# Kernel tuning notes

Measured on AMD Instinct MI355X. Metric: run time of the kernel, lower is better.

The kernel has to match this reference:

```python
import jax, jax.numpy as jnp
import numpy as np

B, N, D = 8, 900, 256
SA_H, CA_H = 8, 8
L, P = 4, 4
FF = 2048
SHAPES = ((128, 128), (64, 64), (32, 32), (16, 16))
STARTS = (0, 16384, 20480, 21504)
S = 21760
D_BAND = (D // 6) * 2   # 84
D_ROPE = 3 * D_BAND     # 252
NF = D_BAND // 2        # 42
EPS = 1e-5


def _ln(x, g, b):
    mu = jnp.mean(x, -1, keepdims=True)
    var = jnp.mean((x - mu) ** 2, -1, keepdims=True)
    return (x - mu) * jax.lax.rsqrt(var + EPS) * g + b


def _rotate_half(x):
    x1 = x[..., 0::2]
    x2 = x[..., 1::2]
    return jnp.stack([-x2, x1], axis=-1).reshape(x.shape)


def _rope(q, k, boxes):
    freqs = 1.0 / (10000.0 ** (jnp.arange(NF, dtype=jnp.float32) / NF))
    cx, cy = boxes[..., 0], boxes[..., 1]
    xy = cx * cy

    def cs(v, f):
        a = v[..., None] * f
        return jnp.repeat(jnp.cos(a), 2, -1), jnp.repeat(jnp.sin(a), 2, -1)

    cx_c, cx_s = cs(cx, freqs)
    cy_c, cy_s = cs(cy, freqs)
    xy_c, xy_s = cs(xy, freqs * 0.1)
    cos = jnp.concatenate([cx_c, cy_c, xy_c], -1)
    sin = jnp.concatenate([cx_s, cy_s, xy_s], -1)

    def app(t):
        a, rest = t[..., :D_ROPE], t[..., D_ROPE:]
        return jnp.concatenate([a * cos + _rotate_half(a) * sin, rest], -1)

    return app(q), app(k)


def _bilinear(img, xy):
    # img: (Hl, Wl, C); xy: (M, 2) normalized in [0,1]
    # torch grid_sample semantics: align_corners=False, zero padding
    Hl, Wl, _ = img.shape
    x = xy[:, 0] * Wl - 0.5
    y = xy[:, 1] * Hl - 0.5
    x0 = jnp.floor(x)
    y0 = jnp.floor(y)
    lx = x - x0
    ly = y - y0
    x0i = x0.astype(jnp.int32)
    y0i = y0.astype(jnp.int32)

    def tap(yi, xi):
        valid = (xi >= 0) & (xi < Wl) & (yi >= 0) & (yi < Hl)
        v = img[jnp.clip(yi, 0, Hl - 1), jnp.clip(xi, 0, Wl - 1)]
        return v * valid[:, None].astype(v.dtype)

    return (tap(y0i, x0i) * ((1 - ly) * (1 - lx))[:, None]
            + tap(y0i, x0i + 1) * ((1 - ly) * lx)[:, None]
            + tap(y0i + 1, x0i) * (ly * (1 - lx))[:, None]
            + tap(y0i + 1, x0i + 1) * (ly * lx)[:, None])


def _forward(tgt, memory, query_pos, ref_boxes, reference_points,
             wq, bq, wk, bk, wv, bv, sa_wo, sa_bo, n1_g, n1_b,
             off_w, off_b, aw_w, aw_b, val_w, val_b, co_w, co_b,
             n2_g, n2_b, ff1_w, ff1_b, ff2_w, ff2_b, n3_g, n3_b):
    dh = D // SA_H
    # --- self attention with ComplexRoPE2D applied pre-projection ---
    q = tgt + query_pos
    k = tgt + query_pos
    q, k = _rope(q, k, ref_boxes)
    qh = (q @ wq + bq).reshape(B, N, SA_H, dh).transpose(0, 2, 1, 3)
    kh = (k @ wk + bk).reshape(B, N, SA_H, dh).transpose(0, 2, 1, 3)
    vh = (tgt @ wv + bv).reshape(B, N, SA_H, dh).transpose(0, 2, 1, 3)
    att = jax.nn.softmax(jnp.einsum('bhqd,bhkd->bhqk', qh, kh) * (dh ** -0.5), axis=-1)
    sa = jnp.einsum('bhqk,bhkd->bhqd', att, vh).transpose(0, 2, 1, 3).reshape(B, N, D)
    tgt = _ln(tgt + sa @ sa_wo + sa_bo, n1_g, n1_b)

    # --- multi-scale deformable cross-attention ---
    cdh = D // CA_H
    q2 = tgt + query_pos
    value = (memory @ val_w + val_b).reshape(B, S, CA_H, cdh)
    off = (q2 @ off_w + off_b).reshape(B, N, CA_H, L, P, 2)
    aw = jax.nn.softmax((q2 @ aw_w + aw_b).reshape(B, N, CA_H, L * P), axis=-1)
    aw = aw.reshape(B, N, CA_H, L, P)
    # offset normalizer is (W, H) per level
    normalizer = jnp.array([[w_, h_] for (h_, w_) in SHAPES], dtype=jnp.float32)
    loc = reference_points[:, :, None, :, None, :] + off / normalizer[None, None, None, :, None, :]
    out = jnp.zeros((B, CA_H, N, cdh), dtype=tgt.dtype)
    for l, (Hl, Wl) in enumerate(SHAPES):
        st = STARTS[l]
        v_l = value[:, st:st + Hl * Wl].reshape(B, Hl, Wl, CA_H, cdh)
        v_l = v_l.transpose(0, 3, 1, 2, 4).reshape(B * CA_H, Hl, Wl, cdh)
        loc_l = loc[:, :, :, l].transpose(0, 2, 1, 3, 4).reshape(B * CA_H, N * P, 2)
        s_l = jax.vmap(_bilinear)(v_l, loc_l).reshape(B, CA_H, N, P, cdh)
        out = out + jnp.einsum('bhnpd,bnhp->bhnd', s_l, aw[:, :, :, l])
    ca = out.transpose(0, 2, 1, 3).reshape(B, N, D) @ co_w + co_b
    tgt = _ln(tgt + ca, n2_g, n2_b)

    # --- FFN ---
    ff = jax.nn.relu(tgt @ ff1_w + ff1_b) @ ff2_w + ff2_b
    return _ln(tgt + ff, n3_g, n3_b)


def setup_inputs() -> dict:
    key = jax.random.key(0)
    ks = jax.random.split(key, 16)

    def wmat(k, shape):
        return jax.random.normal(k, shape, jnp.float32) * 0.02

    z = lambda *s: jnp.zeros(s, jnp.float32)
    o = lambda *s: jnp.ones(s, jnp.float32)
    return dict(
        tgt=jax.random.normal(ks[0], (B, N, D), jnp.float32),
        memory=jax.random.normal(ks[1], (B, S, D), jnp.float32),
        query_pos=jax.random.normal(ks[2], (B, N, D), jnp.float32) * 0.02,
        ref_boxes=jax.random.uniform(ks[3], (B, N, 4), jnp.float32),
        reference_points=jax.random.uniform(ks[4], (B, N, L, 2), jnp.float32),
        wq=wmat(ks[5], (D, D)), bq=z(D),
        wk=wmat(ks[6], (D, D)), bk=z(D),
        wv=wmat(ks[7], (D, D)), bv=z(D),
        sa_wo=wmat(ks[8], (D, D)), sa_bo=z(D),
        n1_g=o(D), n1_b=z(D),
        off_w=wmat(ks[9], (D, CA_H * L * P * 2)), off_b=z(CA_H * L * P * 2),
        aw_w=wmat(ks[10], (D, CA_H * L * P)), aw_b=z(CA_H * L * P),
        val_w=wmat(ks[11], (D, D)), val_b=z(D),
        co_w=wmat(ks[12], (D, D)), co_b=z(D),
        n2_g=o(D), n2_b=z(D),
        ff1_w=wmat(ks[13], (D, FF)), ff1_b=z(FF),
        ff2_w=wmat(ks[14], (FF, D)), ff2_b=z(D),
        n3_g=o(D), n3_b=z(D))


def reference(tgt, memory, query_pos, ref_boxes, reference_points,
              wq, bq, wk, bk, wv, bv, sa_wo, sa_bo, n1_g, n1_b,
              off_w, off_b, aw_w, aw_b, val_w, val_b, co_w, co_b,
              n2_g, n2_b, ff1_w, ff1_b, ff2_w, ff2_b, n3_g, n3_b):
    return _forward(tgt, memory, query_pos, ref_boxes, reference_points,
                    wq, bq, wk, bk, wv, bv, sa_wo, sa_bo, n1_g, n1_b,
                    off_w, off_b, aw_w, aw_b, val_w, val_b, co_w, co_b,
                    n2_g, n2_b, ff1_w, ff1_b, ff2_w, ff2_b, n3_g, n3_b)
```

## Files before the change

### kernel.cpp

```cpp
#include <hip/hip_runtime.h>
#include <hip/hip_bf16.h>
#include <math.h>

#define B_ 8
#define N_ 900
#define D_ 256
#define S_ 21760
#define H_ 8
#define DH 32
#define FF_ 2048
#define NROWS (B_*N_)

typedef __attribute__((ext_vector_type(8))) short bf16x8;
typedef __attribute__((ext_vector_type(4))) float f32x4;

union BU { bf16x8 v; short s[8]; unsigned long long u[2]; };

static __device__ inline short f2bf_s(float x) {
  __hip_bfloat16 h = __float2bfloat16(x);
  return *reinterpret_cast<short*>(&h);
}

__device__ __forceinline__ void gload_lds16(const float* g, float* lds) {
  __builtin_amdgcn_global_load_lds(
      (const __attribute__((address_space(1))) void*)g,
      (__attribute__((address_space(3))) void*)lds, 16, 0, 0);
}

__global__ __launch_bounds__(128) void rope_kernel(
    const float* __restrict__ tgt, const float* __restrict__ qpos,
    const float* __restrict__ boxes, __hip_bfloat16* __restrict__ out)
{
  int row = blockIdx.x;
  int tid = threadIdx.x;
  const float* x = tgt  + (size_t)row * D_;
  const float* p = qpos + (size_t)row * D_;
  float a0 = x[2*tid]   + p[2*tid];
  float a1 = x[2*tid+1] + p[2*tid+1];
  float o0 = a0, o1 = a1;
  if (tid < 126) {
    int band = tid / 42;
    int fi   = tid - band * 42;
    float freq = powf(10000.0f, -(float)fi / 42.0f);
    float cx = boxes[(size_t)row*4 + 0];
    float cy = boxes[(size_t)row*4 + 1];
    float v  = (band == 0) ? cx : (band == 1 ? cy : cx * cy);
    if (band == 2) freq *= 0.1f;
    float ang = v * freq;
    float c = cosf(ang), s = sinf(ang);
    o0 = a0 * c - a1 * s;
    o1 = a1 * c + a0 * s;
  }
  short2 sv = make_short2(f2bf_s(o0), f2bf_s(o1));
  *(short2*)&out[(size_t)row*D_ + 2*tid] = sv;
}

__global__ __launch_bounds__(256) void wtrans_kernel(
    const float* __restrict__ wq, const float* __restrict__ wk,
    const float* __restrict__ wv, const float* __restrict__ sa_wo,
    const float* __restrict__ offw, const float* __restrict__ valw,
    const float* __restrict__ cow, const float* __restrict__ aww,
    const float* __restrict__ ff1w, const float* __restrict__ ff2w,
    short* __restrict__ Wt)
{
  int bid = blockIdx.x;
  const float* W; short* out; int K, N, tile;
  if (bid < 448) {
    int wi = bid >> 6; tile = bid & 63; K = 256; N = 256;
    const float* tab[7] = {wq, wk, wv, sa_wo, offw, valw, cow};
    const int   off[7]  = {0, 65536, 131072, 196608, 262144, 360448, 425984};
    W = tab[wi]; out = Wt + off[wi];
  } else if (bid < 480) {
    tile = bid - 448; K = 256; N = 128; W = aww; out = Wt + 327680;
  } else if (bid < 992) {
    tile = bid - 480; K = 256; N = 2048; W = ff1w; out = Wt + 491520;
  } else {
    tile = bid - 992; K = 2048; N = 256; W = ff2w; out = Wt + 1015808;
  }
  int ntn = N >> 5;
  int tk = tile / ntn, tn = tile - tk * ntn;
  __shared__ float t[32][33];
  int c = threadIdx.x & 31, rr = threadIdx.x >> 5;
  #pragma unroll
  for (int i = 0; i < 4; ++i)
    t[rr + i*8][c] = W[(size_t)(tk*32 + rr + i*8) * N + tn*32 + c];
  __syncthreads();
  #pragma unroll
  for (int i = 0; i < 4; ++i)
    out[(size_t)(tn*32 + rr + i*8) * K + tk*32 + c] = f2bf_s(t[c][rr + i*8]);
}

template<int BM, int KK, bool ABF16, bool A2ADD, bool RELU, int OUTMODE>
__global__ __launch_bounds__(256) void mgemm_kernel(
    const void* __restrict__ Ap, const float* __restrict__ A2p,
    const short* __restrict__ Wt,
    const float* __restrict__ bias, const float* __restrict__ bias2,
    void* __restrict__ Cp, void* __restrict__ Cp2, int M, int N,
    const float* __restrict__ Xres, const float* __restrict__ lng,
    const float* __restrict__ lnb)
{
  constexpr int MS = BM / 16;
  constexpr bool SWAP = (OUTMODE != 2);
  __shared__ short As[BM * 256];
  int tid = threadIdx.x;
  int w = tid >> 6, lane = tid & 63;
  int g = lane >> 4, r = lane & 15;
  int m0 = blockIdx.x * BM;
  int nw = blockIdx.y * 256 + w * 64;
  bool active = nw < N;

  f32x4 acc[MS][4];
  #pragma unroll
  for (int i = 0; i < MS; ++i)
    #pragma unroll
    for (int j = 0; j < 4; ++j) acc[i][j] = (f32x4){0.f,0.f,0.f,0.f};

  for (int kb = 0; kb < KK; kb += 256) {
    if (KK > 256 && kb) __syncthreads();
    #pragma unroll
    for (int i = 0; i < BM/8; ++i) {
      int u = i*256 + tid;
      int row = u >> 5, c8 = u & 31;
      BU pk;
      if (ABF16) {
        pk.v = *(const bf16x8*)((const short*)Ap + (size_t)(m0+row)*KK + kb + c8*8);
      } else {
        const float* ap = (const float*)Ap + (size_t)(m0+row)*KK + kb + c8*8;
        float4 a0 = *(const float4*)ap;
        float4 a1 = *(const float4*)(ap + 4);
        if (A2ADD) {
          const float* a2 = A2p + (size_t)(m0+row)*KK + kb + c8*8;
          float4 b0 = *(const float4*)a2;
          float4 b1 = *(const float4*)(a2 + 4);
          a0.x += b0.x; a0.y += b0.y; a0.z += b0.z; a0.w += b0.w;
          a1.x += b1.x; a1.y += b1.y; a1.z += b1.z; a1.w += b1.w;
        }
        pk.s[0]=f2bf_s(a0.x); pk.s[1]=f2bf_s(a0.y); pk.s[2]=f2bf_s(a0.z); pk.s[3]=f2bf_s(a0.w);
        pk.s[4]=f2bf_s(a1.x); pk.s[5]=f2bf_s(a1.y); pk.s[6]=f2bf_s(a1.z); pk.s[7]=f2bf_s(a1.w);
      }
      int col = (c8*8) ^ ((row & 7) << 3);
      *(bf16x8*)&As[row*256 + col] = pk.v;
    }
    __syncthreads();
    if (active) {
      #pragma unroll
      for (int kk = 0; kk < 8; ++kk) {
        BU bfr[4];
        #pragma unroll
        for (int ns = 0; ns < 4; ++ns) {
          const short* wp = Wt + (size_t)(nw + ns*16 + r)*KK + kb + kk*32;
          bfr[ns].u[0] = *(const unsigned long long*)(wp + 4*g);
          bfr[ns].u[1] = *(const unsigned long long*)(wp + 16 + 4*g);
        }
        #pragma unroll
        for (int ms = 0; ms < MS; ++ms) {
          int row = ms*16 + r;
          int c0 = (kk*32 + g*4)      ^ ((r & 7) << 3);
          int c1 = (kk*32 + 16 + g*4) ^ ((r & 7) << 3);
          BU af;
          af.u[0] = *(const unsigned long long*)&As[row*256 + c0];
          af.u[1] = *(const unsigned long long*)&As[row*256 + c1];
          #pragma unroll
          for (int ns = 0; ns < 4; ++ns) {
            if (SWAP)
              acc[ms][ns] = __builtin_amdgcn_mfma_f32_16x16x32_bf16(
                  bfr[ns].v, af.v, acc[ms][ns], 0, 0, 0);
            else
              acc[ms][ns] = __builtin_amdgcn_mfma_f32_16x16x32_bf16(
                  af.v, bfr[ns].v, acc[ms][ns], 0, 0, 0);
          }
        }
      }
    }
  }

  if (OUTMODE == 5) {
    float vv[MS][16];
    float ps[MS], pq[MS];
    #pragma unroll
    for (int ms = 0; ms < MS; ++ms) {
      ps[ms] = 0.f; pq[ms] = 0.f;
      int m = m0 + ms*16 + r;
      #pragma unroll
      for (int ns = 0; ns < 4; ++ns) {
        int n0 = nw + ns*16 + g*4;
        float4 b4 = *(const float4*)&bias[n0];
        float4 x4 = *(const float4*)&Xres[(size_t)m*256 + n0];
        #pragma unroll
        for (int j = 0; j < 4; ++j) {
          float v = acc[ms][ns][j] + ((const float*)&b4)[j] + ((const float*)&x4)[j];
          vv[ms][ns*4 + j] = v;
          ps[ms] += v; pq[ms] += v*v;
        }
      }
      ps[ms] += __shfl_xor(ps[ms], 16); ps[ms] += __shfl_xor(ps[ms], 32);
      pq[ms] += __shfl_xor(pq[ms], 16); pq[ms] += __shfl_xor(pq[ms], 32);
    }
    __syncthreads();
    float* red = (float*)As;
    if (g == 0) {
      #pragma unroll
      for (int ms = 0; ms < MS; ++ms) {
        red[(ms*16 + r)*8 + w]     = ps[ms];
        red[(ms*16 + r)*8 + 4 + w] = pq[ms];
      }
    }
    __syncthreads();
    #pragma unroll
    for (int ms = 0; ms < MS; ++ms) {
      int rowi = ms*16 + r;
      float ts = red[rowi*8+0]+red[rowi*8+1]+red[rowi*8+2]+red[rowi*8+3];
      float tq = red[rowi*8+4]+red[rowi*8+5]+red[rowi*8+6]+red[rowi*8+7];
      float mu = ts * (1.0f/256.0f);
      float var = tq * (1.0f/256.0f) - mu*mu;
      float rs = rsqrtf(fmaxf(var, 0.f) + 1e-5f);
      int m = m0 + ms*16 + r;
      #pragma unroll
      for (int ns = 0; ns < 4; ++ns) {
        int n0 = nw + ns*16 + g*4;
        float4 g4 = *(const float4*)&lng[n0];
        float4 be = *(const float4*)&lnb[n0];
        float4 ov;
        ov.x = (vv[ms][ns*4+0] - mu)*rs*g4.x + be.x;
        ov.y = (vv[ms][ns*4+1] - mu)*rs*g4.y + be.y;
        ov.z = (vv[ms][ns*4+2] - mu)*rs*g4.z + be.z;
        ov.w = (vv[ms][ns*4+3] - mu)*rs*g4.w + be.w;
        *(float4*)&((float*)Cp)[(size_t)m*256 + n0] = ov;
      }
    }
    return;
  }

  if (!active) return;

  #pragma unroll
  for (int ms = 0; ms < MS; ++ms) {
    #pragma unroll
    for (int ns = 0; ns < 4; ++ns) {
      if (SWAP) {
        int n0 = nw + ns*16 + g*4;
        int m  = m0 + ms*16 + r;
        float4 b4;
        if (OUTMODE == 3 || OUTMODE == 4)
          b4 = (n0 < 256) ? *(const float4*)&bias[n0]
                          : *(const float4*)&bias2[n0 - 256];
        else
          b4 = *(const float4*)&bias[n0];
        float v0 = acc[ms][ns][0] + b4.x;
        float v1 = acc[ms][ns][1] + b4.y;
        float v2 = acc[ms][ns][2] + b4.z;
        float v3 = acc[ms][ns][3] + b4.w;
        if (RELU) {
          v0 = fmaxf(v0, 0.f); v1 = fmaxf(v1, 0.f);
          v2 = fmaxf(v2, 0.f); v3 = fmaxf(v3, 0.f);
        }
        if (OUTMODE == 0) {
          *(float4*)&((float*)Cp)[(size_t)m*N + n0] = make_float4(v0,v1,v2,v3);
        } else if (OUTMODE == 1) {
          short4 sv = make_short4(f2bf_s(v0), f2bf_s(v1), f2bf_s(v2), f2bf_s(v3));
          *(short4*)&((short*)Cp)[(size_t)m*N + n0] = sv;
        } else if (OUTMODE == 3) {
          short4 sv = make_short4(f2bf_s(v0), f2bf_s(v1), f2bf_s(v2), f2bf_s(v3));
          if (n0 < 256) *(short4*)&((short*)Cp )[(size_t)m*256 + n0]       = sv;
          else          *(short4*)&((short*)Cp2)[(size_t)m*256 + (n0-256)] = sv;
        } else {
          float4 fv = make_float4(v0,v1,v2,v3);
          if (n0 < 256) *(float4*)&((float*)Cp )[(size_t)m*256 + n0]       = fv;
          else          *(float4*)&((float*)Cp2)[(size_t)m*128 + (n0-256)] = fv;
        }
      } else {
        int n = nw + ns*16 + r;
        float bsc = bias[n];
        int hh = n >> 5, dd = n & 31;
        int mb = m0 + ms*16 + g*4;
        short4 sv = make_short4(
            f2bf_s(acc[ms][ns][0] + bsc), f2bf_s(acc[ms][ns][1] + bsc),
            f2bf_s(acc[ms][ns][2] + bsc), f2bf_s(acc[ms][ns][3] + bsc));
        int bb = mb / N_, bbe = (mb + 3) / N_;
        if (bb == bbe) {
          int nn = mb - bb * N_;
          *(short4*)&((short*)Cp)[((size_t)((bb*H_ + hh)*DH + dd))*N_ + nn] = sv;
        } else {
          const short* sp = (const short*)&sv;
          #pragma unroll
          for (int j = 0; j < 4; ++j) {
            int m = mb + j;
            int b2 = m / N_, nn = m - b2 * N_;
            ((short*)Cp)[((size_t)((b2*H_ + hh)*DH + dd))*N_ + nn] = sp[j];
          }
        }
      }
    }
  }
}

__global__ __launch_bounds__(256) void vgemm_kernel(
    const float* __restrict__ Ap, const short* __restrict__ Wt,
    const float* __restrict__ bias, short* __restrict__ Cp)
{
  __shared__ float buf[8][1024];
  __shared__ float dump[1024];
  int tid = threadIdx.x;
  int w = tid >> 6, l = tid & 63;
  int g = l >> 4, r = l & 15;
  int nw = w * 64;

  BU wreg[4][8];
  #pragma unroll
  for (int ns = 0; ns < 4; ++ns) {
    const short* wp = Wt + (size_t)(nw + ns*16 + r) * 256;
    #pragma unroll
    for (int kk = 0; kk < 8; ++kk) {
      wreg[ns][kk].u[0] = *(const unsigned long long*)(wp + kk*32 + 4*g);
      wreg[ns][kk].u[1] = *(const unsigned long long*)(wp + kk*32 + 16 + 4*g);
    }
  }
  float4 bs4[4];
  #pragma unroll
  for (int ns = 0; ns < 4; ++ns) bs4[ns] = *(const float4*)&bias[nw + ns*16 + g*4];

  int srow = w*8 + (l >> 3);
  int schunk = (l & 7) ^ (srow & 7);
  const float* gbase = Ap + ((size_t)blockIdx.x*160 + srow) * 256 + schunk*4;

  #pragma unroll
  for (int t = 0; t < 6; ++t)
    gload_lds16(gbase + (t>>3)*8192 + (t&7)*32, &buf[t][w*256]);

  f32x4 acc[2][4];
  #pragma unroll
  for (int i = 0; i < 2; ++i)
    #pragma unroll
    for (int j = 0; j < 4; ++j) acc[i][j] = (f32x4){0.f,0.f,0.f,0.f};

  int bb = blockIdx.x / 136;
  int pixblk = (blockIdx.x % 136) * 160;

  for (int s = 0; s < 5; ++s) {
    #pragma unroll
    for (int c = 0; c < 8; ++c) {
      int t = s*8 + c;
      int tn = t + 6;
      if (tn < 40) gload_lds16(gbase + (tn>>3)*8192 + (tn&7)*32,
                               &buf[(c+6)&7][w*256]);
      else         gload_lds16(gbase, &dump[w*256]);
      asm volatile("s_waitcnt vmcnt(6)" ::: "memory");
      __builtin_amdgcn_s_barrier();
      const float* bp = &buf[c][0];
      #pragma unroll
      for (int ms = 0; ms < 2; ++ms) {
        int row = ms*16 + r;
        const float* rp = bp + row*32;
        float4 f0 = *(const float4*)&rp[((g    ) ^ (row & 7)) * 4];
        float4 f1 = *(const float4*)&rp[((g + 4) ^ (row & 7)) * 4];
        BU af;
        af.s[0]=f2bf_s(f0.x); af.s[1]=f2bf_s(f0.y); af.s[2]=f2bf_s(f0.z); af.s[3]=f2bf_s(f0.w);
        af.s[4]=f2bf_s(f1.x); af.s[5]=f2bf_s(f1.y); af.s[6]=f2bf_s(f1.z); af.s[7]=f2bf_s(f1.w);
        #pragma unroll
        for (int ns = 0; ns < 4; ++ns)
          acc[ms][ns] = __builtin_amdgcn_mfma_f32_16x16x32_bf16(
              wreg[ns][c].v, af.v, acc[ms][ns], 0, 0, 0);
      }
    }
    int pix0 = pixblk + s*32;
    #pragma unroll
    for (int ms = 0; ms < 2; ++ms) {
      #pragma unroll
      for (int ns = 0; ns < 4; ++ns) {
        int pix = pix0 + ms*16 + r;
        int n0  = nw + ns*16 + g*4;
        int hh = n0 >> 5, dd = n0 & 31;
        short4 sv = make_short4(
            f2bf_s(acc[ms][ns][0] + bs4[ns].x),
            f2bf_s(acc[ms][ns][1] + bs4[ns].y),
            f2bf_s(acc[ms][ns][2] + bs4[ns].z),
            f2bf_s(acc[ms][ns][3] + bs4[ns].w));
        *(short4*)&Cp[((size_t)(bb*H_ + hh)*S_ + pix)*32 + dd] = sv;
        acc[ms][ns] = (f32x4){0.f,0.f,0.f,0.f};
      }
    }
  }
}

__global__ __launch_bounds__(64) void mfma_attn_kernel(
    const __hip_bfloat16* __restrict__ Q,
    const __hip_bfloat16* __restrict__ K,
    const __hip_bfloat16* __restrict__ Vt,
    float* __restrict__ O)
{
  const int NQT = 29;
  int wid = blockIdx.x;
  int qt = wid % NQT, bh = wid / NQT;
  int b = bh >> 3, h = bh & 7;
  int lane = threadIdx.x;
  int g = lane >> 4, r = lane & 15;
  int q0 = qt * 32;
  const float scale = 0.17677669529663687f;

  union U { bf16x8 v; short s[8]; unsigned long long u64[2]; };

  U qf[2];
  #pragma unroll
  for (int qq = 0; qq < 2; ++qq) {
    int qrow = min(q0 + qq*16 + r, N_ - 1);
    const __hip_bfloat16* qp = Q + ((size_t)(b*N_ + qrow))*D_ + h*DH;
    qf[qq].u64[0] = *(const unsigned long long*)(qp + 4*g);
    qf[qq].u64[1] = *(const unsigned long long*)(qp + 16 + 4*g);
  }

  f32x4 oaccA[2], oaccB[2];
  #pragma unroll
  for (int qq = 0; qq < 2; ++qq) {
    oaccA[qq] = (f32x4){0.f,0.f,0.f,0.f};
    oaccB[qq] = (f32x4){0.f,0.f,0.f,0.f};
  }
  float m0v = -1e30f, m1v = -1e30f, l0v = 0.f, l1v = 0.f;
  const f32x4 zero = {0.f,0.f,0.f,0.f};

  const __hip_bfloat16* vbase0 = Vt + (size_t)(bh*DH + r) * N_;
  const __hip_bfloat16* vbase1 = Vt + (size_t)(bh*DH + 16 + r) * N_;

  for (int kt = 0; kt < N_; kt += 32) {
    U kf0, kf1;
    {
      int kr0 = min(kt + r, N_ - 1);
      int kr1 = min(kt + 16 + r, N_ - 1);
      const __hip_bfloat16* kp0 = K + ((size_t)(b*N_ + kr0))*D_ + h*DH;
      const __hip_bfloat16* kp1 = K + ((size_t)(b*N_ + kr1))*D_ + h*DH;
      kf0.u64[0] = *(const unsigned long long*)(kp0 + 4*g);
      kf0.u64[1] = *(const unsigned long long*)(kp0 + 16 + 4*g);
      kf1.u64[0] = *(const unsigned long long*)(kp1 + 4*g);
      kf1.u64[1] = *(const unsigned long long*)(kp1 + 16 + 4*g);
    }
    U vf0, vf1;
    vf0.u64[0] = *(const unsigned long long*)(vbase0 + kt + 4*g);
    vf0.u64[1] = *(const unsigned long long*)(vbase0 + kt + 16 + 4*g);
    vf1.u64[0] = *(const unsigned long long*)(vbase1 + kt + 4*g);
    vf1.u64[1] = *(const unsigned long long*)(vbase1 + kt + 16 + 4*g);

    #pragma unroll
    for (int qq = 0; qq < 2; ++qq) {
      f32x4 s0 = __builtin_amdgcn_mfma_f32_16x16x32_bf16(kf0.v, qf[qq].v, zero, 0, 0, 0);
      f32x4 s1 = __builtin_amdgcn_mfma_f32_16x16x32_bf16(kf1.v, qf[qq].v, zero, 0, 0, 0);
      float m = qq ? m1v : m0v;
      float lv = qq ? l1v : l0v;

      float sc[8];
      #pragma unroll
      for (int j = 0; j < 4; ++j) {
        sc[j]   = (kt + 4*g + j      < N_) ? s0[j] * scale : -1e30f;
        sc[4+j] = (kt + 16 + 4*g + j < N_) ? s1[j] * scale : -1e30f;
      }
      float mx = sc[0];
      #pragma unroll
      for (int j = 1; j < 8; ++j) mx = fmaxf(mx, sc[j]);
      mx = fmaxf(mx, __shfl_xor(mx, 16));
      mx = fmaxf(mx, __shfl_xor(mx, 32));

      float mnew = fmaxf(m, mx);
      float corr = __expf(m - mnew);
      float p[8], ps = 0.f;
      #pragma unroll
      for (int j = 0; j < 8; ++j) { p[j] = __expf(sc[j] - mnew); ps += p[j]; }
      ps += __shfl_xor(ps, 16);
      ps += __shfl_xor(ps, 32);
      lv = lv * corr + ps;
      if (qq) { m1v = mnew; l1v = lv; } else { m0v = mnew; l0v = lv; }
      #pragma unroll
      for (int j = 0; j < 4; ++j) { oaccA[qq][j] *= corr; oaccB[qq][j] *= corr; }

      U pf;
      #pragma unroll
      for (int j = 0; j < 8; ++j) pf.s[j] = f2bf_s(p[j]);

      oaccA[qq] = __builtin_amdgcn_mfma_f32_16x16x32_bf16(vf0.v, pf.v, oaccA[qq], 0, 0, 0);
      oaccB[qq] = __builtin_amdgcn_mfma_f32_16x16x32_bf16(vf1.v, pf.v, oaccB[qq], 0, 0, 0);
    }
  }

  #pragma unroll
  for (int qq = 0; qq < 2; ++qq) {
    int qrow = q0 + qq*16 + r;
    if (qrow < N_) {
      float inv = 1.0f / (qq ? l1v : l0v);
      float* op = O + ((size_t)(b*N_ + qrow))*D_ + h*DH;
      #pragma unroll
      for (int j = 0; j < 4; ++j) {
        op[4*g + j]      = oaccA[qq][j] * inv;
        op[16 + 4*g + j] = oaccB[qq][j] * inv;
      }
    }
  }
}

__global__ __launch_bounds__(256) void sample4_kernel(
    const __hip_bfloat16* __restrict__ V, const float* __restrict__ offp,
    const float* __restrict__ awl, const float* __restrict__ refp,
    float* __restrict__ out)
{
  int tid = threadIdx.x;
  int q = tid >> 6, t = tid & 63;
  int row = blockIdx.x * 4 + q;
  int b = row / N_;
  __shared__ float s_aw[4][128];
  __shared__ float s_loc[4][256];
  #pragma unroll
  for (int i = 0; i < 2; ++i)
    s_aw[q][t + i*64] = awl[(size_t)row*128 + t + i*64];
  {
    const float norms[4] = {128.f, 64.f, 32.f, 16.f};
    #pragma unroll
    for (int i = 0; i < 4; ++i) {
      int e = t + i*64;
      int rem = e & 31, li = rem >> 3, ax = rem & 1;
      s_loc[q][e] = refp[((size_t)row*4 + li)*2 + ax]
                  + offp[(size_t)row*256 + e] / norms[li];
    }
  }
  __syncthreads();
  if (t < 8) {
    float mx = -1e30f;
    for (int j = 0; j < 16; ++j) mx = fmaxf(mx, s_aw[q][t*16+j]);
    float sum = 0.f;
    for (int j = 0; j < 16; ++j) sum += __expf(s_aw[q][t*16+j] - mx);
    float inv = 1.0f / sum;
    for (int j = 0; j < 16; ++j)
      s_aw[q][t*16+j] = __expf(s_aw[q][t*16+j] - mx) * inv;
  }
  __syncthreads();
  int h = t >> 3, dq = t & 7;
  const int dims[4]   = {128, 64, 32, 16};
  const int starts[4] = {0, 16384, 20480, 21504};
  const __hip_bfloat16* Vb = V + ((size_t)(b*H_ + h) * S_) * 32 + dq*4;
  float a0 = 0.f, a1 = 0.f, a2 = 0.f, a3 = 0.f;
  #pragma unroll
  for (int l = 0; l < 4; ++l) {
    int Wl = dims[l], st = starts[l];
    #pragma unroll
    for (int p = 0; p < 4; ++p) {
      float lx = s_loc[q][h*32 + l*8 + p*2 + 0];
      float ly = s_loc[q][h*32 + l*8 + p*2 + 1];
      float x = lx * Wl - 0.5f, y = ly * Wl - 0.5f;
      float x0f = floorf(x), y0f = floorf(y);
      float fx = x - x0f, fy = y - y0f;
      int x0 = (int)x0f, y0 = (int)y0f;
      float v0 = 0.f, v1 = 0.f, v2 = 0.f, v3 = 0.f;
      #pragma unroll
      for (int ty = 0; ty < 2; ++ty) {
        int yi = y0 + ty;
        float wy = ty ? fy : (1.f - fy);
        if (yi < 0 || yi >= Wl) continue;
        #pragma unroll
        for (int txi = 0; txi < 2; ++txi) {
          int xi = x0 + txi;
          float wx = txi ? fx : (1.f - fx);
          if (xi < 0 || xi >= Wl) continue;
          unsigned long long vv =
              *(const unsigned long long*)&Vb[(size_t)(st + yi*Wl + xi) * 32];
          float ww = wy * wx;
          v0 += ww * __uint_as_float((unsigned)(vv) << 16);
          v1 += ww * __uint_as_float((unsigned)(vv) & 0xffff0000u);
          v2 += ww * __uint_as_float((unsigned)(vv >> 32) << 16);
          v3 += ww * __uint_as_float((unsigned)(vv >> 32) & 0xffff0000u);
        }
      }
      float aw = s_aw[q][h*16 + l*4 + p];
      a0 += aw * v0; a1 += aw * v1; a2 += aw * v2; a3 += aw * v3;
    }
  }
  float4 res = make_float4(a0, a1, a2, a3);
  *(float4*)&out[(size_t)row*D_ + h*DH + dq*4] = res;
}

extern "C" void kernel_launch(void* const* d_in, const int* in_sizes, int n_in,
                              void* d_out, int out_size, void* d_ws, size_t ws_size,
                              hipStream_t stream)
{
  const float* tgt    = (const float*)d_in[0];
  const float* memory = (const float*)d_in[1];
  const float* qpos   = (const float*)d_in[2];
  const float* boxes  = (const float*)d_in[3];
  const float* refp   = (const float*)d_in[4];
  const float* wq = (const float*)d_in[5];   const float* bq = (const float*)d_in[6];
  const float* wk = (const float*)d_in[7];   const float* bk = (const float*)d_in[8];
  const float* wv = (const float*)d_in[9];   const float* bv = (const float*)d_in[10];
  const float* sa_wo = (const float*)d_in[11]; const float* sa_bo = (const float*)d_in[12];
  const float* n1g = (const float*)d_in[13]; const float* n1b = (const float*)d_in[14];
  const float* off_w = (const float*)d_in[15]; const float* off_b = (const float*)d_in[16];
  const float* aw_w  = (const float*)d_in[17]; const float* aw_b  = (const float*)d_in[18];
  const float* val_w = (const float*)d_in[19]; const float* val_b = (const float*)d_in[20];
  const float* co_w  = (const float*)d_in[21]; const float* co_b  = (const float*)d_in[22];
  const float* n2g = (const float*)d_in[23]; const float* n2b = (const float*)d_in[24];
  const float* ff1_w = (const float*)d_in[25]; const float* ff1_b = (const float*)d_in[26];
  const float* ff2_w = (const float*)d_in[27]; const float* ff2_b = (const float*)d_in[28];
  const float* n3g = (const float*)d_in[29]; const float* n3b = (const float*)d_in[30];

  char* ws = (char*)d_ws;
  size_t NE = (size_t)NROWS * D_;
  __hip_bfloat16* Vv = (__hip_bfloat16*)ws;
  __hip_bfloat16* FFM = (__hip_bfloat16*)ws;
  size_t p = (size_t)B_ * S_ * D_ * sizeof(__hip_bfloat16);
  float* A  = (float*)(ws + p); p += NE*4;
  float* Qb = (float*)(ws + p); p += NE*4;
  float* Kb = (float*)(ws + p); p += NE*4;
  float* Vh = (float*)(ws + p); p += NE*4;
  float* S1 = (float*)(ws + p); p += NE*4;
  float* S2 = (float*)(ws + p); p += NE*4;
  float* T1 = (float*)(ws + p); p += NE*4;
  short* Wt = (short*)((char*)Kb + NE*2);
  float* out = (float*)d_out;
  (void)ws_size; (void)in_sizes; (void)n_in; (void)out_size; (void)S2;

  const short* qk_t  = Wt;
  const short* wv_t  = Wt + 131072;
  const short* sa_t  = Wt + 196608;
  const short* offaw_t = Wt + 262144;
  const short* val_t = Wt + 360448;
  const short* co_t  = Wt + 425984;
  const short* ff1_t = Wt + 491520;
  const short* ff2_t = Wt + 1015808;

  wtrans_kernel<<<1504, 256, 0, stream>>>(wq, wk, wv, sa_wo, off_w, val_w,
                                          co_w, aw_w, ff1_w, ff2_w, Wt);

  rope_kernel<<<NROWS, 128, 0, stream>>>(tgt, qpos, boxes, (__hip_bfloat16*)A);
  mgemm_kernel<32,256,true,false,false,3><<<dim3(225,2), 256, 0, stream>>>(
      A, nullptr, qk_t, bq, bk, Qb, Kb, NROWS, 512, nullptr, nullptr, nullptr);
  mgemm_kernel<32,256,false,false,false,2><<<dim3(225,1), 256, 0, stream>>>(
      tgt, nullptr, wv_t, bv, nullptr, Vh, nullptr, NROWS, 256, nullptr, nullptr, nullptr);
  mfma_attn_kernel<<<29 * B_ * H_, 64, 0, stream>>>(
      (const __hip_bfloat16*)Qb, (const __hip_bfloat16*)Kb,
      (const __hip_bfloat16*)Vh, S1);
  mgemm_kernel<32,256,false,false,false,5><<<dim3(225,1), 256, 0, stream>>>(
      S1, nullptr, sa_t, sa_bo, nullptr, T1, nullptr, NROWS, 256, tgt, n1g, n1b);

  vgemm_kernel<<<1088, 256, 0, stream>>>(memory, val_t, val_b, (short*)Vv);
  mgemm_kernel<32,256,false,true,false,4><<<dim3(225,2), 256, 0, stream>>>(
      T1, qpos, offaw_t, off_b, aw_b, Qb, Kb, NROWS, 384, nullptr, nullptr, nullptr);
  sample4_kernel<<<NROWS/4, 256, 0, stream>>>(Vv, Qb, Kb, refp, S1);
  mgemm_kernel<32,256,false,false,false,5><<<dim3(225,1), 256, 0, stream>>>(
      S1, nullptr, co_t, co_b, nullptr, T1, nullptr, NROWS, 256, T1, n2g, n2b);

  mgemm_kernel<32,256,false,false,true,1><<<dim3(225,8), 256, 0, stream>>>(
      T1, nullptr, ff1_t, ff1_b, nullptr, FFM, nullptr, NROWS, FF_, nullptr, nullptr, nullptr);
  mgemm_kernel<32,2048,true,false,false,5><<<dim3(225,1), 256, 0, stream>>>(
      FFM, nullptr, ff2_t, ff2_b, nullptr, out, nullptr, NROWS, 256, T1, n3g, n3b);
}
```

Measured before the change: 420.0 us.

## Emit bf16 attention outputs and split vgemm columns across eight waves

```diff
diff --git a/kernel.cpp b/kernel.cpp
--- a/kernel.cpp
+++ b/kernel.cpp
@@ -294,7 +294,7 @@
   }
 }
 
-__global__ __launch_bounds__(256) void vgemm_kernel(
+__global__ __launch_bounds__(512) void vgemm_kernel(
     const float* __restrict__ Ap, const short* __restrict__ Wt,
     const float* __restrict__ bias, short* __restrict__ Cp)
 {
@@ -303,11 +303,11 @@
   int tid = threadIdx.x;
   int w = tid >> 6, l = tid & 63;
   int g = l >> 4, r = l & 15;
-  int nw = w * 64;
-
-  BU wreg[4][8];
-  #pragma unroll
-  for (int ns = 0; ns < 4; ++ns) {
+  int nw = w * 32;
+
+  BU wreg[2][8];
+  #pragma unroll
+  for (int ns = 0; ns < 2; ++ns) {
     const short* wp = Wt + (size_t)(nw + ns*16 + r) * 256;
     #pragma unroll
     for (int kk = 0; kk < 8; ++kk) {
@@ -315,23 +315,26 @@
       wreg[ns][kk].u[1] = *(const unsigned long long*)(wp + kk*32 + 16 + 4*g);
     }
   }
-  float4 bs4[4];
-  #pragma unroll
-  for (int ns = 0; ns < 4; ++ns) bs4[ns] = *(const float4*)&bias[nw + ns*16 + g*4];
-
-  int srow = w*8 + (l >> 3);
+  float4 bs4[2];
+  #pragma unroll
+  for (int ns = 0; ns < 2; ++ns) bs4[ns] = *(const float4*)&bias[nw + ns*16 + g*4];
+
+  bool stager = (w < 4);
+  int srow = (w & 3)*8 + (l >> 3);
   int schunk = (l & 7) ^ (srow & 7);
   const float* gbase = Ap + ((size_t)blockIdx.x*160 + srow) * 256 + schunk*4;
 
-  #pragma unroll
-  for (int t = 0; t < 6; ++t)
-    gload_lds16(gbase + (t>>3)*8192 + (t&7)*32, &buf[t][w*256]);
-
-  f32x4 acc[2][4];
+  if (stager) {
+    #pragma unroll
+    for (int t = 0; t < 6; ++t)
+      gload_lds16(gbase + (t>>3)*8192 + (t&7)*32, &buf[t][(w & 3)*256]);
+  }
+
+  f32x4 acc[2][2];
   #pragma unroll
   for (int i = 0; i < 2; ++i)
     #pragma unroll
-    for (int j = 0; j < 4; ++j) acc[i][j] = (f32x4){0.f,0.f,0.f,0.f};
+    for (int j = 0; j < 2; ++j) acc[i][j] = (f32x4){0.f,0.f,0.f,0.f};
 
   int bb = blockIdx.x / 136;
   int pixblk = (blockIdx.x % 136) * 160;
@@ -341,10 +344,12 @@
     for (int c = 0; c < 8; ++c) {
       int t = s*8 + c;
       int tn = t + 6;
-      if (tn < 40) gload_lds16(gbase + (tn>>3)*8192 + (tn&7)*32,
-                               &buf[(c+6)&7][w*256]);
-      else         gload_lds16(gbase, &dump[w*256]);
-      asm volatile("s_waitcnt vmcnt(6)" ::: "memory");
+      if (stager) {
+        if (tn < 40) gload_lds16(gbase + (tn>>3)*8192 + (tn&7)*32,
+                                 &buf[(c+6)&7][(w & 3)*256]);
+        else         gload_lds16(gbase, &dump[(w & 3)*256]);
+        asm volatile("s_waitcnt vmcnt(6)" ::: "memory");
+      }
       __builtin_amdgcn_s_barrier();
       const float* bp = &buf[c][0];
       #pragma unroll
@@ -357,7 +362,7 @@
         af.s[0]=f2bf_s(f0.x); af.s[1]=f2bf_s(f0.y); af.s[2]=f2bf_s(f0.z); af.s[3]=f2bf_s(f0.w);
         af.s[4]=f2bf_s(f1.x); af.s[5]=f2bf_s(f1.y); af.s[6]=f2bf_s(f1.z); af.s[7]=f2bf_s(f1.w);
         #pragma unroll
-        for (int ns = 0; ns < 4; ++ns)
+        for (int ns = 0; ns < 2; ++ns)
           acc[ms][ns] = __builtin_amdgcn_mfma_f32_16x16x32_bf16(
               wreg[ns][c].v, af.v, acc[ms][ns], 0, 0, 0);
       }
@@ -366,7 +371,7 @@
     #pragma unroll
     for (int ms = 0; ms < 2; ++ms) {
       #pragma unroll
-      for (int ns = 0; ns < 4; ++ns) {
+      for (int ns = 0; ns < 2; ++ns) {
         int pix = pix0 + ms*16 + r;
         int n0  = nw + ns*16 + g*4;
         int hh = n0 >> 5, dd = n0 & 31;
@@ -386,7 +391,7 @@
     const __hip_bfloat16* __restrict__ Q,
     const __hip_bfloat16* __restrict__ K,
     const __hip_bfloat16* __restrict__ Vt,
-    float* __restrict__ O)
+    __hip_bfloat16* __restrict__ O)
 {
   const int NQT = 29;
   int wid = blockIdx.x;
@@ -483,12 +488,15 @@
     int qrow = q0 + qq*16 + r;
     if (qrow < N_) {
       float inv = 1.0f / (qq ? l1v : l0v);
-      float* op = O + ((size_t)(b*N_ + qrow))*D_ + h*DH;
-      #pragma unroll
-      for (int j = 0; j < 4; ++j) {
-        op[4*g + j]      = oaccA[qq][j] * inv;
-        op[16 + 4*g + j] = oaccB[qq][j] * inv;
-      }
+      short* op = (short*)(O + ((size_t)(b*N_ + qrow))*D_ + h*DH);
+      short4 sA = make_short4(
+          f2bf_s(oaccA[qq][0]*inv), f2bf_s(oaccA[qq][1]*inv),
+          f2bf_s(oaccA[qq][2]*inv), f2bf_s(oaccA[qq][3]*inv));
+      short4 sB = make_short4(
+          f2bf_s(oaccB[qq][0]*inv), f2bf_s(oaccB[qq][1]*inv),
+          f2bf_s(oaccB[qq][2]*inv), f2bf_s(oaccB[qq][3]*inv));
+      *(short4*)&op[4*g]      = sA;
+      *(short4*)&op[16 + 4*g] = sB;
     }
   }
 }
@@ -496,7 +504,7 @@
 __global__ __launch_bounds__(256) void sample4_kernel(
     const __hip_bfloat16* __restrict__ V, const float* __restrict__ offp,
     const float* __restrict__ awl, const float* __restrict__ refp,
-    float* __restrict__ out)
+    short* __restrict__ out)
 {
   int tid = threadIdx.x;
   int q = tid >> 6, t = tid & 63;
@@ -568,8 +576,8 @@
       a0 += aw * v0; a1 += aw * v1; a2 += aw * v2; a3 += aw * v3;
     }
   }
-  float4 res = make_float4(a0, a1, a2, a3);
-  *(float4*)&out[(size_t)row*D_ + h*DH + dq*4] = res;
+  short4 sv = make_short4(f2bf_s(a0), f2bf_s(a1), f2bf_s(a2), f2bf_s(a3));
+  *(short4*)&out[(size_t)row*D_ + h*DH + dq*4] = sv;
 }
 
 extern "C" void kernel_launch(void* const* d_in, const int* in_sizes, int n_in,
@@ -630,15 +638,15 @@
       tgt, nullptr, wv_t, bv, nullptr, Vh, nullptr, NROWS, 256, nullptr, nullptr, nullptr);
   mfma_attn_kernel<<<29 * B_ * H_, 64, 0, stream>>>(
       (const __hip_bfloat16*)Qb, (const __hip_bfloat16*)Kb,
-      (const __hip_bfloat16*)Vh, S1);
-  mgemm_kernel<32,256,false,false,false,5><<<dim3(225,1), 256, 0, stream>>>(
+      (const __hip_bfloat16*)Vh, (__hip_bfloat16*)S1);
+  mgemm_kernel<32,256,true,false,false,5><<<dim3(225,1), 256, 0, stream>>>(
       S1, nullptr, sa_t, sa_bo, nullptr, T1, nullptr, NROWS, 256, tgt, n1g, n1b);
 
-  vgemm_kernel<<<1088, 256, 0, stream>>>(memory, val_t, val_b, (short*)Vv);
+  vgemm_kernel<<<1088, 512, 0, stream>>>(memory, val_t, val_b, (short*)Vv);
   mgemm_kernel<32,256,false,true,false,4><<<dim3(225,2), 256, 0, stream>>>(
       T1, qpos, offaw_t, off_b, aw_b, Qb, Kb, NROWS, 384, nullptr, nullptr, nullptr);
-  sample4_kernel<<<NROWS/4, 256, 0, stream>>>(Vv, Qb, Kb, refp, S1);
-  mgemm_kernel<32,256,false,false,false,5><<<dim3(225,1), 256, 0, stream>>>(
+  sample4_kernel<<<NROWS/4, 256, 0, stream>>>(Vv, Qb, Kb, refp, (short*)S1);
+  mgemm_kernel<32,256,true,false,false,5><<<dim3(225,1), 256, 0, stream>>>(
       S1, nullptr, co_t, co_b, nullptr, T1, nullptr, NROWS, 256, T1, n2g, n2b);
 
   mgemm_kernel<32,256,false,false,true,1><<<dim3(225,8), 256, 0, stream>>>(
```

Result: no change. 412.8 us (-1.7%).
